# Kernel optimization log

Measured on AMD Instinct MI355X. Metric: run time of the kernel, lower is better.

## Reference

```python
import jax, jax.numpy as jnp
import numpy as np

EPS = 0.001  # variance floor from the original module


def setup_inputs() -> dict:
    key = jax.random.key(0)
    k1, k2, k3, k4, k5, k6 = jax.random.split(key, 6)
    N = 2_000_000  # total anchors
    V = 500_000    # valid (sampled) anchors
    bbox_pred = jax.random.normal(k1, (1, N, 4), dtype=jnp.float32)
    bbox_uncertainty_pred = jax.random.normal(k2, (1, N, 4), dtype=jnp.float32)
    bbox_class = jax.random.normal(k3, (1, N, 2), dtype=jnp.float32)
    gt_bbox = jax.random.normal(k4, (1, N, 4), dtype=jnp.float32)
    gt_anchor_label = jax.random.randint(k5, (1, N), 0, 2, dtype=jnp.int32)
    valid_indices = jnp.sort(jax.random.randint(k6, (1, V), 0, N, dtype=jnp.int32), axis=-1)
    return {
        "bbox_pred": bbox_pred,
        "bbox_uncertainty_pred": bbox_uncertainty_pred,
        "bbox_class": bbox_class,
        "gt_bbox": gt_bbox,
        "gt_anchor_label": gt_anchor_label,
        "valid_indices": valid_indices,
    }


def reference(bbox_pred, bbox_uncertainty_pred, bbox_class, gt_bbox,
              gt_anchor_label, valid_indices):
    vi = valid_indices[0]                       # [V]
    labels = gt_anchor_label[0][vi]             # [V]

    # ---- classification: CrossEntropyLoss (mean over valid anchors) ----
    logits = bbox_class[0][vi]                  # [V, 2]
    logp = jax.nn.log_softmax(logits, axis=-1)
    class_loss = -jnp.mean(jnp.take_along_axis(logp, labels[:, None].astype(jnp.int32), axis=-1))

    pred = bbox_pred[0][vi]                     # [V, 4]
    unc = bbox_uncertainty_pred[0][vi]          # [V, 4]
    gt = gt_bbox[0][vi]                         # [V, 4]
    var = EPS + unc * unc                       # [V, 4]

    pos_term = (0.5 * (pred - gt) ** 2 / var + 0.5 * jnp.log(var)).sum(axis=-1)  # [V]
    neg_term = (1.0 / var).sum(axis=-1)                                          # [V]

    pos = (labels == 1).astype(jnp.float32)     # [V]
    n_pos = pos.sum()
    n_neg = (1.0 - pos).sum()
    reg_loss = (pos_term * pos).sum() / n_pos + (neg_term * (1.0 - pos)).sum() / n_neg

    return class_loss + reg_loss
```

## Files before the change

kernel.cpp:

```cpp
#include <hip/hip_runtime.h>

#define EPS_VAR 0.001f

__device__ __forceinline__ double wave_reduce(double v) {
    #pragma unroll
    for (int off = 32; off > 0; off >>= 1)
        v += __shfl_down(v, off, 64);
    return v;
}

__global__ __launch_bounds__(256) void rpn_pass1(
    const float* __restrict__ pred,
    const float* __restrict__ unc,
    const float* __restrict__ cls,
    const float* __restrict__ gt,
    const int* __restrict__ lab,
    const int* __restrict__ vi,
    int V,
    double* __restrict__ out_part) {

    double s_cls = 0.0, s_pos = 0.0, s_neg = 0.0;
    int n_pos = 0, n_neg = 0;

    const int i = blockIdx.x * 256 + threadIdx.x;
    if (i < V) {
        const int idx = vi[i];

        const float2 lg = *reinterpret_cast<const float2*>(cls + 2ll * idx);
        const float4 u  = *reinterpret_cast<const float4*>(unc + 4ll * idx);
        const int l = lab[idx];

        const float mx = fmaxf(lg.x, lg.y);
        const float d  = fabsf(lg.x - lg.y);
        const float lse = mx + __logf(1.0f + __expf(-d));
        s_cls = (double)(lse - ((l == 1) ? lg.y : lg.x));

        const float v0 = EPS_VAR + u.x * u.x;
        const float v1 = EPS_VAR + u.y * u.y;
        const float v2 = EPS_VAR + u.z * u.z;
        const float v3 = EPS_VAR + u.w * u.w;

        if (l == 1) {
            const float4 p = *reinterpret_cast<const float4*>(pred + 4ll * idx);
            const float4 g = *reinterpret_cast<const float4*>(gt + 4ll * idx);
            const float d0 = p.x - g.x, d1 = p.y - g.y;
            const float d2 = p.z - g.z, d3 = p.w - g.w;
            const float t = 0.5f * (d0 * d0 / v0 + d1 * d1 / v1 +
                                    d2 * d2 / v2 + d3 * d3 / v3)
                          + 0.5f * __logf(v0 * v1 * v2 * v3);
            s_pos = (double)t;
            n_pos = 1;
        } else {
            const float t = 1.0f / v0 + 1.0f / v1 + 1.0f / v2 + 1.0f / v3;
            s_neg = (double)t;
            n_neg = 1;
        }
    }

    __shared__ double sh[4][5];
    const double r0 = wave_reduce(s_cls);
    const double r1 = wave_reduce(s_pos);
    const double r2 = wave_reduce(s_neg);
    const double r3 = wave_reduce((double)n_pos);
    const double r4 = wave_reduce((double)n_neg);

    const int wave = threadIdx.x >> 6;
    if ((threadIdx.x & 63) == 0) {
        sh[wave][0] = r0; sh[wave][1] = r1; sh[wave][2] = r2;
        sh[wave][3] = r3; sh[wave][4] = r4;
    }
    __syncthreads();
    if (threadIdx.x == 0) {
        double a0 = 0, a1 = 0, a2 = 0, a3 = 0, a4 = 0;
        #pragma unroll
        for (int w = 0; w < 4; ++w) {
            a0 += sh[w][0]; a1 += sh[w][1]; a2 += sh[w][2];
            a3 += sh[w][3]; a4 += sh[w][4];
        }
        double* o = out_part + 5ll * blockIdx.x;
        o[0] = a0; o[1] = a1; o[2] = a2; o[3] = a3; o[4] = a4;
    }
}

__global__ __launch_bounds__(256) void rpn_pass2(
    const double* __restrict__ part, int nb, int V, float* __restrict__ out) {

    double a0 = 0, a1 = 0, a2 = 0, a3 = 0, a4 = 0;
    for (int i = threadIdx.x; i < nb; i += 256) {
        const double* p = part + 5ll * i;
        a0 += p[0]; a1 += p[1]; a2 += p[2]; a3 += p[3]; a4 += p[4];
    }

    __shared__ double sh[4][5];
    a0 = wave_reduce(a0);
    a1 = wave_reduce(a1);
    a2 = wave_reduce(a2);
    a3 = wave_reduce(a3);
    a4 = wave_reduce(a4);

    const int wave = threadIdx.x >> 6;
    if ((threadIdx.x & 63) == 0) {
        sh[wave][0] = a0; sh[wave][1] = a1; sh[wave][2] = a2;
        sh[wave][3] = a3; sh[wave][4] = a4;
    }
    __syncthreads();
    if (threadIdx.x == 0) {
        double t0 = 0, t1 = 0, t2 = 0, t3 = 0, t4 = 0;
        #pragma unroll
        for (int w = 0; w < 4; ++w) {
            t0 += sh[w][0]; t1 += sh[w][1]; t2 += sh[w][2];
            t3 += sh[w][3]; t4 += sh[w][4];
        }
        const double class_loss = t0 / (double)V;
        const double reg_loss = t1 / t3 + t2 / t4;
        out[0] = (float)(class_loss + reg_loss);
    }
}

extern "C" void kernel_launch(void* const* d_in, const int* in_sizes, int n_in,
                              void* d_out, int out_size, void* d_ws, size_t ws_size,
                              hipStream_t stream) {
    const float* pred = (const float*)d_in[0];
    const float* unc  = (const float*)d_in[1];
    const float* cls  = (const float*)d_in[2];
    const float* gt   = (const float*)d_in[3];
    const int*   lab  = (const int*)d_in[4];
    const int*   vi   = (const int*)d_in[5];
    const int V = in_sizes[5];

    const int NB = (V + 255) / 256;
    double* part = (double*)d_ws;

    rpn_pass1<<<NB, 256, 0, stream>>>(pred, unc, cls, gt, lab, vi, V, part);
    rpn_pass2<<<1, 256, 0, stream>>>(part, NB, V, (float*)d_out);
}
```

Measured before the change: 25.52 us.

## Process four anchors per thread with unconditional gathers and branchless accumulation

Each thread now handles four consecutive valid indices, loaded as one int4, and issues all label, logit, uncertainty, pred and gt gathers up front to raise memory-level parallelism. The label-dependent branch is replaced by computing both the positive and negative terms and selecting, so pred and gt are always loaded even for negatives. The negative count is derived as V minus the positive count, which removes one reduction and shrinks the partials. The cost is extra gather traffic for negative anchors and a quarter as many blocks.

```diff
diff --git a/kernel.cpp b/kernel.cpp
--- a/kernel.cpp
+++ b/kernel.cpp
@@ -7,6 +7,32 @@
     for (int off = 32; off > 0; off >>= 1)
         v += __shfl_down(v, off, 64);
     return v;
+}
+
+__device__ __forceinline__ void accum_elem(
+    int l, float2 lg, float4 u, float4 p, float4 g,
+    double& s_cls, double& s_pos, double& s_neg, int& n_pos) {
+    const float mx = fmaxf(lg.x, lg.y);
+    const float dd = fabsf(lg.x - lg.y);
+    const float lse = mx + __logf(1.0f + __expf(-dd));
+    const bool pos = (l == 1);
+    s_cls += (double)(lse - (pos ? lg.y : lg.x));
+
+    const float v0 = EPS_VAR + u.x * u.x;
+    const float v1 = EPS_VAR + u.y * u.y;
+    const float v2 = EPS_VAR + u.z * u.z;
+    const float v3 = EPS_VAR + u.w * u.w;
+
+    const float d0 = p.x - g.x, d1 = p.y - g.y;
+    const float d2 = p.z - g.z, d3 = p.w - g.w;
+    const float pos_t = 0.5f * (d0 * d0 / v0 + d1 * d1 / v1 +
+                                d2 * d2 / v2 + d3 * d3 / v3)
+                      + 0.5f * __logf(v0 * v1 * v2 * v3);
+    const float neg_t = 1.0f / v0 + 1.0f / v1 + 1.0f / v2 + 1.0f / v3;
+
+    s_pos += (double)(pos ? pos_t : 0.0f);
+    s_neg += (double)(pos ? 0.0f : neg_t);
+    n_pos += pos ? 1 : 0;
 }
 
 __global__ __launch_bounds__(256) void rpn_pass1(
@@ -20,99 +46,99 @@
     double* __restrict__ out_part) {
 
     double s_cls = 0.0, s_pos = 0.0, s_neg = 0.0;
-    int n_pos = 0, n_neg = 0;
+    int n_pos = 0;
 
-    const int i = blockIdx.x * 256 + threadIdx.x;
-    if (i < V) {
-        const int idx = vi[i];
+    const int t = blockIdx.x * 256 + threadIdx.x;
+    const int base = t * 4;
 
-        const float2 lg = *reinterpret_cast<const float2*>(cls + 2ll * idx);
-        const float4 u  = *reinterpret_cast<const float4*>(unc + 4ll * idx);
-        const int l = lab[idx];
+    if (base + 3 < V) {
+        const int4 ii = *reinterpret_cast<const int4*>(vi + base);
+        const int i0 = ii.x, i1 = ii.y, i2 = ii.z, i3 = ii.w;
 
-        const float mx = fmaxf(lg.x, lg.y);
-        const float d  = fabsf(lg.x - lg.y);
-        const float lse = mx + __logf(1.0f + __expf(-d));
-        s_cls = (double)(lse - ((l == 1) ? lg.y : lg.x));
+        const int l0 = lab[i0], l1 = lab[i1], l2 = lab[i2], l3 = lab[i3];
+        const float2 a0 = *reinterpret_cast<const float2*>(cls + 2ll * i0);
+        const float2 a1 = *reinterpret_cast<const float2*>(cls + 2ll * i1);
+        const float2 a2 = *reinterpret_cast<const float2*>(cls + 2ll * i2);
+        const float2 a3 = *reinterpret_cast<const float2*>(cls + 2ll * i3);
+        const float4 u0 = *reinterpret_cast<const float4*>(unc + 4ll * i0);
+        const float4 u1 = *reinterpret_cast<const float4*>(unc + 4ll * i1);
+        const float4 u2 = *reinterpret_cast<const float4*>(unc + 4ll * i2);
+        const float4 u3 = *reinterpret_cast<const float4*>(unc + 4ll * i3);
+        const float4 p0 = *reinterpret_cast<const float4*>(pred + 4ll * i0);
+        const float4 p1 = *reinterpret_cast<const float4*>(pred + 4ll * i1);
+        const float4 p2 = *reinterpret_cast<const float4*>(pred + 4ll * i2);
+        const float4 p3 = *reinterpret_cast<const float4*>(pred + 4ll * i3);
+        const float4 g0 = *reinterpret_cast<const float4*>(gt + 4ll * i0);
+        const float4 g1 = *reinterpret_cast<const float4*>(gt + 4ll * i1);
+        const float4 g2 = *reinterpret_cast<const float4*>(gt + 4ll * i2);
+        const float4 g3 = *reinterpret_cast<const float4*>(gt + 4ll * i3);
 
-        const float v0 = EPS_VAR + u.x * u.x;
-        const float v1 = EPS_VAR + u.y * u.y;
-        const float v2 = EPS_VAR + u.z * u.z;
-        const float v3 = EPS_VAR + u.w * u.w;
-
-        if (l == 1) {
+        accum_elem(l0, a0, u0, p0, g0, s_cls, s_pos, s_neg, n_pos);
+        accum_elem(l1, a1, u1, p1, g1, s_cls, s_pos, s_neg, n_pos);
+        accum_elem(l2, a2, u2, p2, g2, s_cls, s_pos, s_neg, n_pos);
+        accum_elem(l3, a3, u3, p3, g3, s_cls, s_pos, s_neg, n_pos);
+    } else {
+        for (int i = base; i < V && i < base + 4; ++i) {
+            const int idx = vi[i];
+            const int l = lab[idx];
+            const float2 a = *reinterpret_cast<const float2*>(cls + 2ll * idx);
+            const float4 u = *reinterpret_cast<const float4*>(unc + 4ll * idx);
             const float4 p = *reinterpret_cast<const float4*>(pred + 4ll * idx);
             const float4 g = *reinterpret_cast<const float4*>(gt + 4ll * idx);
-            const float d0 = p.x - g.x, d1 = p.y - g.y;
-            const float d2 = p.z - g.z, d3 = p.w - g.w;
-            const float t = 0.5f * (d0 * d0 / v0 + d1 * d1 / v1 +
-                                    d2 * d2 / v2 + d3 * d3 / v3)
-                          + 0.5f * __logf(v0 * v1 * v2 * v3);
-            s_pos = (double)t;
-            n_pos = 1;
-        } else {
-            const float t = 1.0f / v0 + 1.0f / v1 + 1.0f / v2 + 1.0f / v3;
-            s_neg = (double)t;
-            n_neg = 1;
+            accum_elem(l, a, u, p, g, s_cls, s_pos, s_neg, n_pos);
         }
     }
 
-    __shared__ double sh[4][5];
+    __shared__ double sh[4][4];
     const double r0 = wave_reduce(s_cls);
     const double r1 = wave_reduce(s_pos);
     const double r2 = wave_reduce(s_neg);
     const double r3 = wave_reduce((double)n_pos);
-    const double r4 = wave_reduce((double)n_neg);
 
     const int wave = threadIdx.x >> 6;
     if ((threadIdx.x & 63) == 0) {
-        sh[wave][0] = r0; sh[wave][1] = r1; sh[wave][2] = r2;
-        sh[wave][3] = r3; sh[wave][4] = r4;
+        sh[wave][0] = r0; sh[wave][1] = r1; sh[wave][2] = r2; sh[wave][3] = r3;
     }
     __syncthreads();
     if (threadIdx.x == 0) {
-        double a0 = 0, a1 = 0, a2 = 0, a3 = 0, a4 = 0;
+        double a0 = 0, a1 = 0, a2 = 0, a3 = 0;
         #pragma unroll
         for (int w = 0; w < 4; ++w) {
-            a0 += sh[w][0]; a1 += sh[w][1]; a2 += sh[w][2];
-            a3 += sh[w][3]; a4 += sh[w][4];
+            a0 += sh[w][0]; a1 += sh[w][1]; a2 += sh[w][2]; a3 += sh[w][3];
         }
-        double* o = out_part + 5ll * blockIdx.x;
-        o[0] = a0; o[1] = a1; o[2] = a2; o[3] = a3; o[4] = a4;
+        double* o = out_part + 4ll * blockIdx.x;
+        o[0] = a0; o[1] = a1; o[2] = a2; o[3] = a3;
     }
 }
 
 __global__ __launch_bounds__(256) void rpn_pass2(
     const double* __restrict__ part, int nb, int V, float* __restrict__ out) {
 
-    double a0 = 0, a1 = 0, a2 = 0, a3 = 0, a4 = 0;
+    double a0 = 0, a1 = 0, a2 = 0, a3 = 0;
     for (int i = threadIdx.x; i < nb; i += 256) {
-        const double* p = part + 5ll * i;
-        a0 += p[0]; a1 += p[1]; a2 += p[2]; a3 += p[3]; a4 += p[4];
+        const double* p = part + 4ll * i;
+        a0 += p[0]; a1 += p[1]; a2 += p[2]; a3 += p[3];
     }
 
-    __shared__ double sh[4][5];
+    __shared__ double sh[4][4];
     a0 = wave_reduce(a0);
     a1 = wave_reduce(a1);
     a2 = wave_reduce(a2);
     a3 = wave_reduce(a3);
-    a4 = wave_reduce(a4);
 
     const int wave = threadIdx.x >> 6;
     if ((threadIdx.x & 63) == 0) {
-        sh[wave][0] = a0; sh[wave][1] = a1; sh[wave][2] = a2;
-        sh[wave][3] = a3; sh[wave][4] = a4;
+        sh[wave][0] = a0; sh[wave][1] = a1; sh[wave][2] = a2; sh[wave][3] = a3;
     }
     __syncthreads();
     if (threadIdx.x == 0) {
-        double t0 = 0, t1 = 0, t2 = 0, t3 = 0, t4 = 0;
+        double t0 = 0, t1 = 0, t2 = 0, t3 = 0;
         #pragma unroll
         for (int w = 0; w < 4; ++w) {
-            t0 += sh[w][0]; t1 += sh[w][1]; t2 += sh[w][2];
-            t3 += sh[w][3]; t4 += sh[w][4];
+            t0 += sh[w][0]; t1 += sh[w][1]; t2 += sh[w][2]; t3 += sh[w][3];
         }
         const double class_loss = t0 / (double)V;
-        const double reg_loss = t1 / t3 + t2 / t4;
+        const double reg_loss = t1 / t3 + t2 / ((double)V - t3);
         out[0] = (float)(class_loss + reg_loss);
     }
 }
@@ -128,7 +154,7 @@
     const int*   vi   = (const int*)d_in[5];
     const int V = in_sizes[5];
 
-    const int NB = (V + 255) / 256;
+    const int NB = (V + 1023) / 1024;
     double* part = (double*)d_ws;
 
     rpn_pass1<<<NB, 256, 0, stream>>>(pred, unc, cls, gt, lab, vi, V, part);
```

After: 33.09 us. 1.3x slower.
